# Kernel optimization log

Hardware: AMD Instinct MI355X
Metric: run time of the kernel (lower is better)

The kernel has to match this reference:

```python
import jax, jax.numpy as jnp
import numpy as np

DT, TAU = 0.02, 0.1


def setup_inputs() -> dict:
    key = jax.random.key(0)
    ks = jax.random.split(key, 7)
    B, T, IN, H = 64, 2048, 64, 256
    return {
        "x0": jax.random.normal(ks[0], (B, H), jnp.float32),
        "I": jax.random.normal(ks[1], (B, T, IN), jnp.float32),
        "W_in": jax.random.normal(ks[2], (H, IN), jnp.float32) / np.sqrt(IN),
        "W_rec": jax.random.normal(ks[3], (H, H), jnp.float32) / np.sqrt(H),
        "b": jax.random.normal(ks[4], (H,), jnp.float32) * 0.1,
        "Wout": jax.random.normal(ks[5], (2, H), jnp.float32) / np.sqrt(H),
        "bout": jax.random.normal(ks[6], (2,), jnp.float32) * 0.1,
    }


def reference(x0, I, W_in, W_rec, b, Wout, bout):
    # Continuous-time leaky RNN, forward-Euler integration.
    # u_{t+1} = (1 - dt/tau) * u_t + (dt/tau) * (tanh(u_t) @ W_rec^T + I_t @ W_in^T + b)
    alpha = DT / TAU

    def step(u, I_t):
        r = jnp.tanh(u)                                   # [B, H]
        drive = r @ W_rec.T + I_t @ W_in.T + b            # [B, H]
        u_new = (1.0 - alpha) * u + alpha * drive
        return u_new, u_new

    I_tbf = jnp.swapaxes(I, 0, 1)                         # [T, B, IN]
    _, us = jax.lax.scan(step, x0, I_tbf)                 # [T, B, H]
    u = jnp.swapaxes(us, 0, 1)                            # [B, T, H]
    y = u @ Wout.T + bout                                 # [B, T, 2] linear readout
    return u, y
```

## Files before the change

### kernel.cpp

```cpp
#include <hip/hip_runtime.h>

#define BB 64
#define TT 2048
#define INW 64
#define HH 256
#define NXB 512
#define RPB ((BB * TT) / NXB)
#define NW 8
#define KC (HH / NW)
#define PSTR 260

typedef float v2f __attribute__((ext_vector_type(2)));

__device__ __forceinline__ v2f fma2(v2f a, v2f b, v2f c) {
#if __has_builtin(__builtin_elementwise_fma)
    return __builtin_elementwise_fma(a, b, c);
#else
    v2f r; r.x = __builtin_fmaf(a.x, b.x, c.x); r.y = __builtin_fmaf(a.y, b.y, c.y); return r;
#endif
}

__device__ __forceinline__ float fast_tanh(float x) {
    float e = __expf(2.0f * x);
    return 1.0f - 2.0f / (e + 1.0f);
}

__device__ __forceinline__ void lds_barrier() {
    asm volatile("s_waitcnt lgkmcnt(0)" ::: "memory");
    __builtin_amdgcn_s_barrier();
    __builtin_amdgcn_sched_barrier(0);
}

__global__ __launch_bounds__(256)
void xprep(const float* __restrict__ I,
           const float* __restrict__ W_in,
           const float* __restrict__ bias,
           float* __restrict__ X)
{
    const int h = threadIdx.x;
    const size_t row0 = (size_t)blockIdx.x * RPB;

    v2f w[32];
    {
        const float4* wp = (const float4*)(W_in + (size_t)h * INW);
        #pragma unroll
        for (int i = 0; i < 16; ++i) {
            float4 a = wp[i];
            w[2*i]     = (v2f){a.x, a.y};
            w[2*i + 1] = (v2f){a.z, a.w};
        }
    }
    const float bv = bias[h];

    for (int r = 0; r < RPB; ++r) {
        const float4* ip = (const float4*)(I + (row0 + r) * INW);
        v2f acc0 = {0.f, 0.f}, acc1 = {0.f, 0.f};
        #pragma unroll
        for (int i = 0; i < 16; ++i) {
            float4 iv = ip[i];
            acc0 = fma2(w[2*i],     (v2f){iv.x, iv.y}, acc0);
            acc1 = fma2(w[2*i + 1], (v2f){iv.z, iv.w}, acc1);
        }
        v2f s = acc0 + acc1;
        X[(row0 + r) * HH + h] = s.x + s.y + bv;
    }
}

__global__ __launch_bounds__(512, 1)
void rnn_scan(const float* __restrict__ x0,
              const float* __restrict__ W_rec,
              float* uX)
{
    __shared__ __align__(16) float r_buf[HH];
    __shared__ __align__(16) float xbuf[2][HH];
    __shared__ __align__(16) float part[NW][PSTR];

    const int b    = blockIdx.x;
    const int tid  = threadIdx.x;
    const int lane = tid & 63;
    const int w    = tid >> 6;
    const int k0   = w * KC;
    const int h0   = lane * 4;
    const int il   = tid - 256;

    v2f wr[4][16];
    #pragma unroll
    for (int m = 0; m < 4; ++m) {
        const float4* wp = (const float4*)(W_rec + (size_t)(h0 + m) * HH + k0);
        #pragma unroll
        for (int i = 0; i < 8; ++i) {
            float4 a = wp[i];
            wr[m][2*i]     = (v2f){a.x, a.y};
            wr[m][2*i + 1] = (v2f){a.z, a.w};
        }
    }

    float u = 0.0f;
    if (tid < HH) {
        u = x0[(size_t)b * HH + tid];
        r_buf[tid] = fast_tanh(u);
    }
    if (tid < 64)
        ((float4*)&xbuf[0][0])[tid] = ((const float4*)(uX + (size_t)b * TT * HH))[tid];
    float4 x_next = {0.f, 0.f, 0.f, 0.f};
    if ((unsigned)il < 64u)
        x_next = ((const float4*)(uX + ((size_t)b * TT + 1) * HH))[il];
    __syncthreads();

    const float4* rb4 = (const float4*)&r_buf[k0];

    for (int t = 0; t < TT; ++t) {
        float4 x_fut = {0.f, 0.f, 0.f, 0.f};
        if ((unsigned)il < 64u && (t + 2) < TT)
            x_fut = ((const float4*)(uX + ((size_t)b * TT + t + 2) * HH))[il];

        v2f a0[4] = {{0.f,0.f},{0.f,0.f},{0.f,0.f},{0.f,0.f}};
        v2f a1[4] = {{0.f,0.f},{0.f,0.f},{0.f,0.f},{0.f,0.f}};
        #pragma unroll
        for (int i = 0; i < 8; ++i) {
            float4 r4 = rb4[i];
            v2f r01 = (v2f){r4.x, r4.y}, r23 = (v2f){r4.z, r4.w};
            #pragma unroll
            for (int m = 0; m < 4; ++m) {
                a0[m] = fma2(wr[m][2*i],     r01, a0[m]);
                a1[m] = fma2(wr[m][2*i + 1], r23, a1[m]);
            }
        }
        float4 dv;
        { v2f s = a0[0] + a1[0]; dv.x = s.x + s.y; }
        { v2f s = a0[1] + a1[1]; dv.y = s.x + s.y; }
        { v2f s = a0[2] + a1[2]; dv.z = s.x + s.y; }
        { v2f s = a0[3] + a1[3]; dv.w = s.x + s.y; }
        *(float4*)&part[w][h0] = dv;
        lds_barrier();

        if (tid < HH) {
            float d = (((part[0][tid] + part[1][tid]) + (part[2][tid] + part[3][tid])) +
                       ((part[4][tid] + part[5][tid]) + (part[6][tid] + part[7][tid])))
                      + xbuf[t & 1][tid];
            u = 0.8f * u + 0.2f * d;
            uX[((size_t)b * TT + t) * HH + tid] = u;
            r_buf[tid] = fast_tanh(u);
        }
        if ((unsigned)il < 64u && (t + 1) < TT)
            *(float4*)&xbuf[(t + 1) & 1][4 * il] = x_next;
        x_next = x_fut;
        lds_barrier();
    }
}

__global__ __launch_bounds__(256)
void readout(const float* __restrict__ u,
             const float* __restrict__ Wout,
             const float* __restrict__ bout,
             float* __restrict__ y)
{
    const int wid  = threadIdx.x >> 6;
    const int lane = threadIdx.x & 63;
    const size_t row = (size_t)blockIdx.x * 4 + wid;

    float4 uv = ((const float4*)(u + row * HH))[lane];
    float4 w0 = ((const float4*)Wout)[lane];
    float4 w1 = ((const float4*)(Wout + HH))[lane];

    float acc0 = uv.x * w0.x + uv.y * w0.y + uv.z * w0.z + uv.w * w0.w;
    float acc1 = uv.x * w1.x + uv.y * w1.y + uv.z * w1.z + uv.w * w1.w;

    #pragma unroll
    for (int m = 32; m >= 1; m >>= 1) {
        acc0 += __shfl_xor(acc0, m, 64);
        acc1 += __shfl_xor(acc1, m, 64);
    }
    if (lane == 0) {
        y[row * 2 + 0] = acc0 + bout[0];
        y[row * 2 + 1] = acc1 + bout[1];
    }
}

extern "C" void kernel_launch(void* const* d_in, const int* in_sizes, int n_in,
                              void* d_out, int out_size, void* d_ws, size_t ws_size,
                              hipStream_t stream) {
    const float* x0    = (const float*)d_in[0];
    const float* I     = (const float*)d_in[1];
    const float* W_in  = (const float*)d_in[2];
    const float* W_rec = (const float*)d_in[3];
    const float* bias  = (const float*)d_in[4];
    const float* Wout  = (const float*)d_in[5];
    const float* bout  = (const float*)d_in[6];

    float* u_out = (float*)d_out;
    float* y_out = u_out + (size_t)BB * TT * HH;

    xprep<<<NXB, 256, 0, stream>>>(I, W_in, bias, u_out);
    rnn_scan<<<BB, 512, 0, stream>>>(x0, W_rec, u_out);
    readout<<<(BB * TT) / 4, 256, 0, stream>>>(u_out, Wout, bout, y_out);
}
```

Before: 1.761 ms.

## Process two batch rows per scan block sharing W_rec registers across 16 waves

The recurrent scan kernel now handles two batch elements per block with 1024 threads split into 16 K-chunks, so each W_rec register slice is reused for two sequences. Only 32 blocks are launched instead of 64. The aim is to amortize weight-register loads and the per-step barrier cost over two rows, which doubles the per-step FMA work per block. The cost is a larger 16-way partial-sum reduction, more LDS traffic per step, and fewer CUs in use.

```diff
diff --git a/kernel.cpp b/kernel.cpp
--- a/kernel.cpp
+++ b/kernel.cpp
@@ -6,12 +6,25 @@
 #define HH 256
 #define NXB 512
 #define RPB ((BB * TT) / NXB)
-#define NW 8
-#define KC (HH / NW)
-#define PSTR 260
+#define BPB 2
+#define NBLK (BB / BPB)
+#define NKC 16
+#define KCW 16
+#define PSTR 264
 
 typedef float v2f __attribute__((ext_vector_type(2)));
-
+typedef float v4f __attribute__((ext_vector_type(4)));
+
+__device__ __forceinline__ v4f fma4(v4f a, v4f b, v4f c) {
+#if __has_builtin(__builtin_elementwise_fma)
+    return __builtin_elementwise_fma(a, b, c);
+#else
+    v4f r;
+    r.x = __builtin_fmaf(a.x, b.x, c.x); r.y = __builtin_fmaf(a.y, b.y, c.y);
+    r.z = __builtin_fmaf(a.z, b.z, c.z); r.w = __builtin_fmaf(a.w, b.w, c.w);
+    return r;
+#endif
+}
 __device__ __forceinline__ v2f fma2(v2f a, v2f b, v2f c) {
 #if __has_builtin(__builtin_elementwise_fma)
     return __builtin_elementwise_fma(a, b, c);
@@ -66,85 +79,100 @@
     }
 }
 
-__global__ __launch_bounds__(512, 1)
+__global__ __launch_bounds__(1024, 1)
 void rnn_scan(const float* __restrict__ x0,
               const float* __restrict__ W_rec,
               float* uX)
 {
-    __shared__ __align__(16) float r_buf[HH];
-    __shared__ __align__(16) float xbuf[2][HH];
-    __shared__ __align__(16) float part[NW][PSTR];
-
-    const int b    = blockIdx.x;
+    __shared__ __align__(16) float r_buf[BPB][HH];
+    __shared__ __align__(16) float xbuf[2][BPB][HH];
+    __shared__ __align__(16) float part[BPB][NKC][PSTR];
+
+    const int b0   = blockIdx.x * BPB;
     const int tid  = threadIdx.x;
     const int lane = tid & 63;
     const int w    = tid >> 6;
-    const int k0   = w * KC;
-    const int h0   = lane * 4;
-    const int il   = tid - 256;
-
-    v2f wr[4][16];
+    const int k0   = w * KCW;
+    const int h0   = lane << 2;
+
+    const int cb = tid >> 8;
+    const int ch = tid & 255;
+    const int sid = tid - 512;
+    const int sb  = (sid >> 6) & 1;
+    const int sj  = sid & 63;
+
+    v4f w4[4][4];
     #pragma unroll
     for (int m = 0; m < 4; ++m) {
-        const float4* wp = (const float4*)(W_rec + (size_t)(h0 + m) * HH + k0);
-        #pragma unroll
-        for (int i = 0; i < 8; ++i) {
-            float4 a = wp[i];
-            wr[m][2*i]     = (v2f){a.x, a.y};
-            wr[m][2*i + 1] = (v2f){a.z, a.w};
-        }
+        const v4f* wp = (const v4f*)(W_rec + (size_t)(h0 + m) * HH + k0);
+        #pragma unroll
+        for (int i = 0; i < 4; ++i) w4[m][i] = wp[i];
     }
 
     float u = 0.0f;
-    if (tid < HH) {
-        u = x0[(size_t)b * HH + tid];
-        r_buf[tid] = fast_tanh(u);
-    }
-    if (tid < 64)
-        ((float4*)&xbuf[0][0])[tid] = ((const float4*)(uX + (size_t)b * TT * HH))[tid];
-    float4 x_next = {0.f, 0.f, 0.f, 0.f};
-    if ((unsigned)il < 64u)
-        x_next = ((const float4*)(uX + ((size_t)b * TT + 1) * HH))[il];
+    if (tid < 2 * HH) {
+        u = x0[(size_t)(b0 + cb) * HH + ch];
+        r_buf[cb][ch] = fast_tanh(u);
+    }
+    v4f x_next = {0.f, 0.f, 0.f, 0.f};
+    if ((unsigned)sid < 128u) {
+        ((v4f*)&xbuf[0][sb][0])[sj] = ((const v4f*)(uX + (size_t)(b0 + sb) * TT * HH))[sj];
+        x_next = ((const v4f*)(uX + ((size_t)(b0 + sb) * TT + 1) * HH))[sj];
+    }
     __syncthreads();
 
-    const float4* rb4 = (const float4*)&r_buf[k0];
+    const v4f* rb0 = (const v4f*)&r_buf[0][k0];
+    const v4f* rb1 = (const v4f*)&r_buf[1][k0];
 
     for (int t = 0; t < TT; ++t) {
-        float4 x_fut = {0.f, 0.f, 0.f, 0.f};
-        if ((unsigned)il < 64u && (t + 2) < TT)
-            x_fut = ((const float4*)(uX + ((size_t)b * TT + t + 2) * HH))[il];
-
-        v2f a0[4] = {{0.f,0.f},{0.f,0.f},{0.f,0.f},{0.f,0.f}};
-        v2f a1[4] = {{0.f,0.f},{0.f,0.f},{0.f,0.f},{0.f,0.f}};
-        #pragma unroll
-        for (int i = 0; i < 8; ++i) {
-            float4 r4 = rb4[i];
-            v2f r01 = (v2f){r4.x, r4.y}, r23 = (v2f){r4.z, r4.w};
+        v4f x_fut = {0.f, 0.f, 0.f, 0.f};
+        if ((unsigned)sid < 128u && (t + 2) < TT)
+            x_fut = ((const v4f*)(uX + ((size_t)(b0 + sb) * TT + t + 2) * HH))[sj];
+
+        v4f a0[4] = {{0,0,0,0},{0,0,0,0},{0,0,0,0},{0,0,0,0}};
+        v4f a1[4] = {{0,0,0,0},{0,0,0,0},{0,0,0,0},{0,0,0,0}};
+        #pragma unroll
+        for (int i = 0; i < 4; ++i) {
+            v4f r0 = rb0[i], r1 = rb1[i];
             #pragma unroll
             for (int m = 0; m < 4; ++m) {
-                a0[m] = fma2(wr[m][2*i],     r01, a0[m]);
-                a1[m] = fma2(wr[m][2*i + 1], r23, a1[m]);
+                a0[m] = fma4(w4[m][i], r0, a0[m]);
+                a1[m] = fma4(w4[m][i], r1, a1[m]);
             }
         }
-        float4 dv;
-        { v2f s = a0[0] + a1[0]; dv.x = s.x + s.y; }
-        { v2f s = a0[1] + a1[1]; dv.y = s.x + s.y; }
-        { v2f s = a0[2] + a1[2]; dv.z = s.x + s.y; }
-        { v2f s = a0[3] + a1[3]; dv.w = s.x + s.y; }
-        *(float4*)&part[w][h0] = dv;
+        v4f dv0, dv1;
+        dv0.x = (a0[0].x + a0[0].y) + (a0[0].z + a0[0].w);
+        dv0.y = (a0[1].x + a0[1].y) + (a0[1].z + a0[1].w);
+        dv0.z = (a0[2].x + a0[2].y) + (a0[2].z + a0[2].w);
+        dv0.w = (a0[3].x + a0[3].y) + (a0[3].z + a0[3].w);
+        dv1.x = (a1[0].x + a1[0].y) + (a1[0].z + a1[0].w);
+        dv1.y = (a1[1].x + a1[1].y) + (a1[1].z + a1[1].w);
+        dv1.z = (a1[2].x + a1[2].y) + (a1[2].z + a1[2].w);
+        dv1.w = (a1[3].x + a1[3].y) + (a1[3].z + a1[3].w);
+        *(v4f*)&part[0][w][h0] = dv0;
+        *(v4f*)&part[1][w][h0] = dv1;
         lds_barrier();
 
-        if (tid < HH) {
-            float d = (((part[0][tid] + part[1][tid]) + (part[2][tid] + part[3][tid])) +
-                       ((part[4][tid] + part[5][tid]) + (part[6][tid] + part[7][tid])))
-                      + xbuf[t & 1][tid];
+        if (tid < 2 * HH) {
+            float p0  = part[cb][ 0][ch], p1  = part[cb][ 1][ch];
+            float p2  = part[cb][ 2][ch], p3  = part[cb][ 3][ch];
+            float p4  = part[cb][ 4][ch], p5  = part[cb][ 5][ch];
+            float p6  = part[cb][ 6][ch], p7  = part[cb][ 7][ch];
+            float p8  = part[cb][ 8][ch], p9  = part[cb][ 9][ch];
+            float p10 = part[cb][10][ch], p11 = part[cb][11][ch];
+            float p12 = part[cb][12][ch], p13 = part[cb][13][ch];
+            float p14 = part[cb][14][ch], p15 = part[cb][15][ch];
+            float d = ((((p0 + p1) + (p2 + p3)) + ((p4 + p5) + (p6 + p7))) +
+                       (((p8 + p9) + (p10 + p11)) + ((p12 + p13) + (p14 + p15))))
+                      + xbuf[t & 1][cb][ch];
             u = 0.8f * u + 0.2f * d;
-            uX[((size_t)b * TT + t) * HH + tid] = u;
-            r_buf[tid] = fast_tanh(u);
-        }
-        if ((unsigned)il < 64u && (t + 1) < TT)
-            *(float4*)&xbuf[(t + 1) & 1][4 * il] = x_next;
-        x_next = x_fut;
+            uX[((size_t)(b0 + cb) * TT + t) * HH + ch] = u;
+            r_buf[cb][ch] = fast_tanh(u);
+        }
+        if ((unsigned)sid < 128u && (t + 1) < TT) {
+            ((v4f*)&xbuf[(t + 1) & 1][sb][0])[sj] = x_next;
+            x_next = x_fut;
+        }
         lds_barrier();
     }
 }
@@ -192,6 +220,6 @@
     float* y_out = u_out + (size_t)BB * TT * HH;
 
     xprep<<<NXB, 256, 0, stream>>>(I, W_in, bias, u_out);
-    rnn_scan<<<BB, 512, 0, stream>>>(x0, W_rec, u_out);
+    rnn_scan<<<NBLK, 1024, 0, stream>>>(x0, W_rec, u_out);
     readout<<<(BB * TT) / 4, 256, 0, stream>>>(u_out, Wout, bout, y_out);
 }
```

Result: slower. 3.240 ms (+84.0%).
